# Optimization experiments

Hardware: AMD Instinct MI355X
Metric: run time of the kernel (lower is better)

The kernel has to match this reference:

```python
import jax, jax.numpy as jnp
import numpy as np

IN_FEATURES_LS = (32, 64, 128, 256)
OUT_FEATURES = 1024
B, T = 16, 4096


def setup_inputs() -> dict:
    key = jax.random.key(0)
    k_x, k_idx, k_w, k_b = jax.random.split(key, 4)
    n = len(IN_FEATURES_LS)
    x = jax.random.normal(k_x, (B, T, OUT_FEATURES), dtype=jnp.float32)
    # per-row declared feature size, drawn from the configured list
    branch_idx = jax.random.randint(k_idx, (B, T), 0, n)
    in_feat_size = jnp.array(IN_FEATURES_LS, dtype=jnp.int32)[branch_idx]
    # kaiming_uniform_(a=sqrt(5)) on (n, out, out): fan_in = out, bound = 1/sqrt(fan_in)
    bound_w = 1.0 / np.sqrt(OUT_FEATURES)
    weight = jax.random.uniform(k_w, (n, OUT_FEATURES, OUT_FEATURES), dtype=jnp.float32,
                                minval=-bound_w, maxval=bound_w)
    bound_b = 1.0 / np.sqrt(OUT_FEATURES)
    bias = jax.random.uniform(k_b, (n, OUT_FEATURES), dtype=jnp.float32,
                              minval=-bound_b, maxval=bound_b)
    return {"x": x, "in_feat_size": in_feat_size, "weight": weight, "bias": bias}


def reference(x, in_feat_size, weight, bias):
    # Loop over the small fixed set of feature-size branches (matches original).
    out = jnp.zeros(x.shape[:-1] + (OUT_FEATURES,), dtype=x.dtype)
    for idx, feat_size in enumerate(IN_FEATURES_LS):
        mask = (in_feat_size == feat_size)[..., None].astype(x.dtype)  # [B,T,1]
        y = jnp.einsum('oi,bti->bto', weight[idx], x) + bias[idx]
        out = out + mask * y
    return out
```

## Files before the change

### kernel.cpp

```cpp
#include <hip/hip_runtime.h>
#include <hip/hip_bf16.h>

#define OUTF 1024
#define NROWS 65536
#define NBR 4
#define BM 128
#define BN 128
#define BK 64
#define LDT 72

typedef __attribute__((ext_vector_type(8))) short short8;
typedef __attribute__((ext_vector_type(4))) float f32x4;

__device__ inline unsigned short f2bf(float f) {
    return __builtin_bit_cast(unsigned short, (__bf16)f);
}

__device__ inline void gload_lds16(const void* g, void* l) {
    __builtin_amdgcn_global_load_lds(
        (const __attribute__((address_space(1))) void*)g,
        (__attribute__((address_space(3))) void*)l, 16, 0, 0);
}

__global__ void k_count(const int* __restrict__ feat, int* __restrict__ cnt) {
    __shared__ int lc[NBR];
    int tid = threadIdx.x;
    if (tid < NBR) lc[tid] = 0;
    __syncthreads();
    int r = blockIdx.x * 256 + tid;
    int b = 26 - __clz(feat[r]);
    atomicAdd(&lc[b], 1);
    __syncthreads();
    if (tid < NBR && lc[tid]) atomicAdd(&cnt[tid], lc[tid]);
}

__global__ void k_prefix(int* __restrict__ ws) {
    if (threadIdx.x == 0) {
        int s = 0;
        for (int b = 0; b < NBR; b++) { ws[4 + b] = s; s += ws[b]; ws[8 + b] = 0; }
    }
}

__global__ void k_fill(const int* __restrict__ feat, int* __restrict__ ws,
                       int* __restrict__ rowlist) {
    int tid = threadIdx.x;
    int lane = tid & 63;
    int r = blockIdx.x * 256 + tid;
    int b = 26 - __clz(feat[r]);
    #pragma unroll
    for (int bb = 0; bb < NBR; bb++) {
        unsigned long long mask = __ballot(b == bb);
        int leader = __ffsll((long long)mask) - 1;
        int cntw = __popcll(mask);
        int basepos = 0;
        if (lane == leader) basepos = atomicAdd(&ws[8 + bb], cntw);
        basepos = __shfl(basepos, leader < 0 ? 0 : leader);
        if (b == bb) {
            int prefix = __popcll(mask & ((1ull << lane) - 1ull));
            rowlist[ws[4 + bb] + basepos + prefix] = r;
        }
    }
}

__global__ void k_convw(const float* __restrict__ w, unsigned short* __restrict__ wb) {
    int i = ((int)blockIdx.x * 256 + (int)threadIdx.x) * 4;
    const float4 v = *reinterpret_cast<const float4*>(w + i);
    ushort4 o;
    o.x = f2bf(v.x); o.y = f2bf(v.y); o.z = f2bf(v.z); o.w = f2bf(v.w);
    *reinterpret_cast<ushort4*>(wb + i) = o;
}

__global__ void k_convx(const float* __restrict__ x, const int* __restrict__ rowlist,
                        unsigned short* __restrict__ xb) {
    int idx = ((int)blockIdx.x * 256 + (int)threadIdx.x) << 3;
    int row = idx >> 10;
    int col = idx & (OUTF - 1);
    int src = rowlist[row];
    const float4* s = reinterpret_cast<const float4*>(x + (size_t)src * OUTF + col);
    float4 v0 = s[0], v1 = s[1];
    short8 o;
    o[0] = (short)f2bf(v0.x); o[1] = (short)f2bf(v0.y);
    o[2] = (short)f2bf(v0.z); o[3] = (short)f2bf(v0.w);
    o[4] = (short)f2bf(v1.x); o[5] = (short)f2bf(v1.y);
    o[6] = (short)f2bf(v1.z); o[7] = (short)f2bf(v1.w);
    *reinterpret_cast<short8*>(xb + idx) = o;
}

__global__ __launch_bounds__(256, 3)
void k_gemm2(const unsigned short* __restrict__ xb,
             const unsigned short* __restrict__ wb,
             const float* __restrict__ bias,
             const int* __restrict__ ws_i,
             const int* __restrict__ rowlist,
             float* __restrict__ out) {
    __shared__ unsigned short As[BM][BK];
    __shared__ unsigned short Bs[BN][BK];

    const int nwg = (int)gridDim.x;
    const int d = (int)blockIdx.x;
    const int wg = (d & 7) * (nwg >> 3) + (d >> 3);
    const int mtile = wg >> 3;
    const int ntile = wg & 7;

    int branch = -1, lt = 0, cnt = 0, rbase = 0;
    int t = mtile;
    #pragma unroll
    for (int b = 0; b < NBR; b++) {
        if (branch < 0) {
            int c = ws_i[b];
            int nt = (c + BM - 1) >> 7;
            if (t < nt) { branch = b; lt = t; cnt = c; rbase = ws_i[4 + b]; }
            else t -= nt;
        }
    }
    if (branch < 0) return;

    const int tid = threadIdx.x;
    const int lane = tid & 63;
    const int w = tid >> 6;
    const int wm = (w & 1) << 6;
    const int wn = (w >> 1) << 6;
    const int n0 = ntile * BN;
    const int row0 = rbase + lt * BM;

    const int lr = lane >> 3;
    const int lc = (lane & 7) << 3;
    const unsigned short* gA = xb + (size_t)(row0 + w * 32 + lr) * OUTF + lc;
    const unsigned short* gB = wb + ((size_t)branch << 20) + (size_t)(n0 + w * 32 + lr) * OUTF + lc;
    unsigned short* lA = &As[w * 32][0];
    unsigned short* lB = &Bs[w * 32][0];

    f32x4 acc[4][4];
    #pragma unroll
    for (int i = 0; i < 4; i++)
        #pragma unroll
        for (int j = 0; j < 4; j++)
            acc[i][j] = (f32x4){0.f, 0.f, 0.f, 0.f};

    for (int k0 = 0; k0 < OUTF; k0 += BK) {
        #pragma unroll
        for (int i = 0; i < 4; i++) {
            gload_lds16(gA + (size_t)i * 8 * OUTF + k0, lA + i * 8 * BK);
            gload_lds16(gB + (size_t)i * 8 * OUTF + k0, lB + i * 8 * BK);
        }
        __syncthreads();
        #pragma unroll
        for (int kk = 0; kk < BK; kk += 32) {
            const int krd = kk + (lane >> 4) * 8;
            short8 af[4], bfr[4];
            #pragma unroll
            for (int i = 0; i < 4; i++)
                af[i] = *reinterpret_cast<const short8*>(&As[wm + i * 16 + (lane & 15)][krd]);
            #pragma unroll
            for (int i = 0; i < 4; i++)
                bfr[i] = *reinterpret_cast<const short8*>(&Bs[wn + i * 16 + (lane & 15)][krd]);
            #pragma unroll
            for (int i = 0; i < 4; i++)
                #pragma unroll
                for (int j = 0; j < 4; j++)
                    acc[i][j] = __builtin_amdgcn_mfma_f32_16x16x32_bf16(af[i], bfr[j], acc[i][j], 0, 0, 0);
        }
        __syncthreads();
    }

    const int ccol = lane & 15;
    const int crow = (lane >> 4) << 2;
    float bv[4];
    const float* bp = bias + branch * OUTF + n0 + wn;
    #pragma unroll
    for (int fn = 0; fn < 4; fn++) bv[fn] = bp[fn * 16 + ccol];
    #pragma unroll
    for (int fm = 0; fm < 4; fm++) {
        #pragma unroll
        for (int j = 0; j < 4; j++) {
            int gm = lt * BM + wm + fm * 16 + crow + j;
            if (gm < cnt) {
                int orow = rowlist[rbase + gm];
                float* orp = out + (size_t)orow * OUTF + n0 + wn;
                #pragma unroll
                for (int fn = 0; fn < 4; fn++)
                    orp[fn * 16 + ccol] = acc[fm][fn][j] + bv[fn];
            }
        }
    }
}

template <bool USE_WB>
__global__ __launch_bounds__(256, 3)
void k_gemm_fb(const float* __restrict__ x,
               const unsigned short* __restrict__ wb,
               const float* __restrict__ wf,
               const float* __restrict__ bias,
               const int* __restrict__ ws_i,
               const int* __restrict__ rowlist,
               float* __restrict__ out) {
    __shared__ unsigned short As[BM][LDT];
    __shared__ unsigned short Bs[BN][LDT];

    int t = (int)blockIdx.x;
    int branch = -1, ltile = 0, cnt = 0, rbase = 0;
    #pragma unroll
    for (int b = 0; b < NBR; b++) {
        if (branch < 0) {
            int c = ws_i[b];
            int nt = (c + BM - 1) >> 7;
            if (t < nt) { branch = b; ltile = t; cnt = c; rbase = ws_i[4 + b]; }
            else t -= nt;
        }
    }
    if (branch < 0) return;

    const int tid = threadIdx.x;
    const int lane = tid & 63;
    const int wid = tid >> 6;
    const int wm = (wid & 1) << 6;
    const int wn = (wid >> 1) << 6;
    const int n0 = (int)blockIdx.y * BN;

    const int srow = tid >> 1;
    const int scol = (tid & 1) << 5;

    const int gmrow = ltile * BM + srow;
    const int grow = (gmrow < cnt) ? rowlist[rbase + gmrow] : -1;
    const float* xsrc = x + (size_t)(grow < 0 ? 0 : grow) * OUTF + scol;
    const unsigned short* wbsrc = wb + ((size_t)branch << 20) + (size_t)(n0 + srow) * OUTF + scol;
    const float* wfsrc = wf + ((size_t)branch << 20) + (size_t)(n0 + srow) * OUTF + scol;

    f32x4 acc[4][4];
    #pragma unroll
    for (int i = 0; i < 4; i++)
        #pragma unroll
        for (int j = 0; j < 4; j++)
            acc[i][j] = (f32x4){0.f, 0.f, 0.f, 0.f};

    for (int k0 = 0; k0 < OUTF; k0 += BK) {
        {
            unsigned short* dst = &As[srow][scol];
            if (grow >= 0) {
                const float4* s4 = reinterpret_cast<const float4*>(xsrc + k0);
                #pragma unroll
                for (int i = 0; i < 8; i++) {
                    float4 v = s4[i];
                    ushort4 o;
                    o.x = f2bf(v.x); o.y = f2bf(v.y); o.z = f2bf(v.z); o.w = f2bf(v.w);
                    reinterpret_cast<ushort4*>(dst)[i] = o;
                }
            } else {
                ushort4 z; z.x = z.y = z.z = z.w = 0;
                #pragma unroll
                for (int i = 0; i < 8; i++) reinterpret_cast<ushort4*>(dst)[i] = z;
            }
        }
        {
            unsigned short* dst = &Bs[srow][scol];
            if (USE_WB) {
                const int4* s4 = reinterpret_cast<const int4*>(wbsrc + k0);
                #pragma unroll
                for (int i = 0; i < 4; i++) reinterpret_cast<int4*>(dst)[i] = s4[i];
            } else {
                const float4* s4 = reinterpret_cast<const float4*>(wfsrc + k0);
                #pragma unroll
                for (int i = 0; i < 8; i++) {
                    float4 v = s4[i];
                    ushort4 o;
                    o.x = f2bf(v.x); o.y = f2bf(v.y); o.z = f2bf(v.z); o.w = f2bf(v.w);
                    reinterpret_cast<ushort4*>(dst)[i] = o;
                }
            }
        }
        __syncthreads();
        #pragma unroll
        for (int kk = 0; kk < BK; kk += 32) {
            const int krd = kk + (lane >> 4) * 8;
            short8 af[4], bf_[4];
            #pragma unroll
            for (int i = 0; i < 4; i++)
                af[i] = *reinterpret_cast<const short8*>(&As[wm + i * 16 + (lane & 15)][krd]);
            #pragma unroll
            for (int i = 0; i < 4; i++)
                bf_[i] = *reinterpret_cast<const short8*>(&Bs[wn + i * 16 + (lane & 15)][krd]);
            #pragma unroll
            for (int i = 0; i < 4; i++)
                #pragma unroll
                for (int j = 0; j < 4; j++)
                    acc[i][j] = __builtin_amdgcn_mfma_f32_16x16x32_bf16(af[i], bf_[j], acc[i][j], 0, 0, 0);
        }
        __syncthreads();
    }

    const int ccol = lane & 15;
    const int crow = (lane >> 4) << 2;
    float bv[4];
    const float* bp = bias + branch * OUTF + n0 + wn;
    #pragma unroll
    for (int fn = 0; fn < 4; fn++) bv[fn] = bp[fn * 16 + ccol];
    #pragma unroll
    for (int fm = 0; fm < 4; fm++) {
        #pragma unroll
        for (int j = 0; j < 4; j++) {
            int gm = ltile * BM + wm + fm * 16 + crow + j;
            if (gm < cnt) {
                int orow = rowlist[rbase + gm];
                float* orp = out + (size_t)orow * OUTF + n0 + wn;
                #pragma unroll
                for (int fn = 0; fn < 4; fn++)
                    orp[fn * 16 + ccol] = acc[fm][fn][j] + bv[fn];
            }
        }
    }
}

extern "C" void kernel_launch(void* const* d_in, const int* in_sizes, int n_in,
                              void* d_out, int out_size, void* d_ws, size_t ws_size,
                              hipStream_t stream) {
    const float* x = (const float*)d_in[0];
    const int* feat = (const int*)d_in[1];
    const float* w = (const float*)d_in[2];
    const float* bias = (const float*)d_in[3];
    float* out = (float*)d_out;

    char* ws = (char*)d_ws;
    int* ws_i = (int*)ws;
    int* rowlist = (int*)(ws + 256);
    const size_t WB_OFF = (size_t)512 << 10;
    const size_t XB_OFF = (size_t)16 << 20;
    unsigned short* wb = (unsigned short*)(ws + WB_OFF);
    unsigned short* xb = (unsigned short*)(ws + XB_OFF);
    const size_t need_wb = WB_OFF + (size_t)NBR * OUTF * OUTF * 2;
    const size_t need_full = XB_OFF + (size_t)(NROWS + 128) * OUTF * 2;

    hipMemsetAsync(ws_i, 0, 64, stream);
    k_count<<<NROWS / 256, 256, 0, stream>>>(feat, ws_i);
    k_prefix<<<1, 64, 0, stream>>>(ws_i);
    k_fill<<<NROWS / 256, 256, 0, stream>>>(feat, ws_i, rowlist);

    if (ws_size >= need_full) {
        k_convw<<<(NBR * OUTF * OUTF) / (256 * 4), 256, 0, stream>>>(w, wb);
        k_convx<<<(NROWS * (OUTF / 8)) / 256, 256, 0, stream>>>(x, rowlist, xb);
        const int nwg = (NROWS / BM + NBR) * (OUTF / BN);
        k_gemm2<<<nwg, 256, 0, stream>>>(xb, wb, bias, ws_i, rowlist, out);
    } else {
        dim3 grid(NROWS / BM + NBR, OUTF / BN);
        if (ws_size >= need_wb) {
            k_convw<<<(NBR * OUTF * OUTF) / (256 * 4), 256, 0, stream>>>(w, wb);
            k_gemm_fb<true><<<grid, 256, 0, stream>>>(x, wb, w, bias, ws_i, rowlist, out);
        } else {
            k_gemm_fb<false><<<grid, 256, 0, stream>>>(x, wb, w, bias, ws_i, rowlist, out);
        }
    }
}
```

Before: 365.6 us.

## Fuse x bf16 conversion into a larger double-buffered 256x256 GEMM tile

Removes the separate gather-and-convert pass over x. The GEMM now loads fp32 rows through rowlist, converts them to bf16 in registers and writes them to swizzled LDS. Tiles grow to 256x256 with 512 threads and 128KB of dynamic LDS, double-buffered so the next K-slab loads while MFMAs run, with setprio around the MFMA phases. This saves a full write and read of the bf16 copy of x, at the cost of lower occupancy, heavier register pressure and more padding waste on the ragged per-branch tiles.

```diff
diff --git a/kernel.cpp b/kernel.cpp
--- a/kernel.cpp
+++ b/kernel.cpp
@@ -4,10 +4,6 @@
 #define OUTF 1024
 #define NROWS 65536
 #define NBR 4
-#define BM 128
-#define BN 128
-#define BK 64
-#define LDT 72
 
 typedef __attribute__((ext_vector_type(8))) short short8;
 typedef __attribute__((ext_vector_type(4))) float f32x4;
@@ -15,11 +11,18 @@
 __device__ inline unsigned short f2bf(float f) {
     return __builtin_bit_cast(unsigned short, (__bf16)f);
 }
-
 __device__ inline void gload_lds16(const void* g, void* l) {
     __builtin_amdgcn_global_load_lds(
         (const __attribute__((address_space(1))) void*)g,
         (__attribute__((address_space(3))) void*)l, 16, 0, 0);
+}
+__device__ inline short8 pack8(float4 a, float4 b) {
+    short8 o;
+    o[0] = (short)f2bf(a.x); o[1] = (short)f2bf(a.y);
+    o[2] = (short)f2bf(a.z); o[3] = (short)f2bf(a.w);
+    o[4] = (short)f2bf(b.x); o[5] = (short)f2bf(b.y);
+    o[6] = (short)f2bf(b.z); o[7] = (short)f2bf(b.w);
+    return o;
 }
 
 __global__ void k_count(const int* __restrict__ feat, int* __restrict__ cnt) {
@@ -70,47 +73,30 @@
     *reinterpret_cast<ushort4*>(wb + i) = o;
 }
 
-__global__ void k_convx(const float* __restrict__ x, const int* __restrict__ rowlist,
-                        unsigned short* __restrict__ xb) {
-    int idx = ((int)blockIdx.x * 256 + (int)threadIdx.x) << 3;
-    int row = idx >> 10;
-    int col = idx & (OUTF - 1);
-    int src = rowlist[row];
-    const float4* s = reinterpret_cast<const float4*>(x + (size_t)src * OUTF + col);
-    float4 v0 = s[0], v1 = s[1];
-    short8 o;
-    o[0] = (short)f2bf(v0.x); o[1] = (short)f2bf(v0.y);
-    o[2] = (short)f2bf(v0.z); o[3] = (short)f2bf(v0.w);
-    o[4] = (short)f2bf(v1.x); o[5] = (short)f2bf(v1.y);
-    o[6] = (short)f2bf(v1.z); o[7] = (short)f2bf(v1.w);
-    *reinterpret_cast<short8*>(xb + idx) = o;
-}
-
-__global__ __launch_bounds__(256, 3)
-void k_gemm2(const unsigned short* __restrict__ xb,
+__global__ __launch_bounds__(512, 2)
+void k_gemm3(const float* __restrict__ x,
              const unsigned short* __restrict__ wb,
              const float* __restrict__ bias,
              const int* __restrict__ ws_i,
              const int* __restrict__ rowlist,
              float* __restrict__ out) {
-    __shared__ unsigned short As[BM][BK];
-    __shared__ unsigned short Bs[BN][BK];
-
+    extern __shared__ char lds[];
+
+    const int d = (int)blockIdx.x;
     const int nwg = (int)gridDim.x;
-    const int d = (int)blockIdx.x;
-    const int wg = (d & 7) * (nwg >> 3) + (d >> 3);
-    const int mtile = wg >> 3;
-    const int ntile = wg & 7;
+    const int work = (d & 7) * (nwg >> 3) + (d >> 3);
+    const int mtile = work >> 2;
+    const int ntile = work & 3;
 
     int branch = -1, lt = 0, cnt = 0, rbase = 0;
-    int t = mtile;
+    int t_ = mtile;
     #pragma unroll
     for (int b = 0; b < NBR; b++) {
         if (branch < 0) {
             int c = ws_i[b];
-            int nt = (c + BM - 1) >> 7;
-            if (t < nt) { branch = b; lt = t; cnt = c; rbase = ws_i[4 + b]; }
-            else t -= nt;
+            int nt = (c + 255) >> 8;
+            if (t_ < nt) { branch = b; lt = t_; cnt = c; rbase = ws_i[4 + b]; }
+            else t_ -= nt;
         }
     }
     if (branch < 0) return;
@@ -118,49 +104,140 @@
     const int tid = threadIdx.x;
     const int lane = tid & 63;
     const int w = tid >> 6;
-    const int wm = (w & 1) << 6;
-    const int wn = (w >> 1) << 6;
-    const int n0 = ntile * BN;
-    const int row0 = rbase + lt * BM;
-
-    const int lr = lane >> 3;
-    const int lc = (lane & 7) << 3;
-    const unsigned short* gA = xb + (size_t)(row0 + w * 32 + lr) * OUTF + lc;
-    const unsigned short* gB = wb + ((size_t)branch << 20) + (size_t)(n0 + w * 32 + lr) * OUTF + lc;
-    unsigned short* lA = &As[w * 32][0];
-    unsigned short* lB = &Bs[w * 32][0];
-
-    f32x4 acc[4][4];
-    #pragma unroll
-    for (int i = 0; i < 4; i++)
-        #pragma unroll
-        for (int j = 0; j < 4; j++)
-            acc[i][j] = (f32x4){0.f, 0.f, 0.f, 0.f};
-
-    for (int k0 = 0; k0 < OUTF; k0 += BK) {
+    const int wm = (w >> 2) * 128;
+    const int wn = (w & 3) * 64;
+    const int n0 = ntile * 256;
+
+    const float4* pA[4];
+    const char* gB[4];
+    const int row0 = rbase + lt * 256;
+    #pragma unroll
+    for (int i = 0; i < 4; i++) {
+        const int Dl = i * 8192 + w * 1024 + lane * 16;
+        const int row = Dl >> 7;
+        const int colb = (Dl & 127) ^ ((row & 7) << 4);
+        int idx = row0 + row;
+        int grow = rowlist[idx < NROWS ? idx : 0];
+        pA[i] = reinterpret_cast<const float4*>(x + (size_t)grow * OUTF + (colb >> 1));
+        gB[i] = reinterpret_cast<const char*>(wb + ((size_t)branch << 20) + (size_t)(n0 + row) * OUTF) + colb;
+    }
+
+    f32x4 acc[8][4];
+    #pragma unroll
+    for (int i = 0; i < 8; i++)
+        #pragma unroll
+        for (int j = 0; j < 4; j++) acc[i][j] = (f32x4){0.f, 0.f, 0.f, 0.f};
+
+    const int klane = (lane >> 4) << 4;
+    const int swz = (lane & 7) << 4;
+    const int arow = wm + (lane & 15);
+    const int brow = wn + (lane & 15);
+
+    {
+        char* A0 = lds;
+        char* B0 = lds + 32768;
         #pragma unroll
         for (int i = 0; i < 4; i++) {
-            gload_lds16(gA + (size_t)i * 8 * OUTF + k0, lA + i * 8 * BK);
-            gload_lds16(gB + (size_t)i * 8 * OUTF + k0, lB + i * 8 * BK);
-        }
+            float4 a0 = pA[i][0], a1 = pA[i][1];
+            const int Dl = i * 8192 + w * 1024 + lane * 16;
+            *reinterpret_cast<short8*>(A0 + Dl) = pack8(a0, a1);
+        }
+        #pragma unroll
+        for (int i = 0; i < 4; i++)
+            gload_lds16(gB[i], B0 + i * 8192 + w * 1024);
         __syncthreads();
-        #pragma unroll
-        for (int kk = 0; kk < BK; kk += 32) {
-            const int krd = kk + (lane >> 4) * 8;
-            short8 af[4], bfr[4];
+    }
+
+    short8 af[8], bfr[2];
+    int cur = 0;
+
+    for (int t = 0; t < 16; ++t) {
+        const int nb = cur ^ 1;
+        const bool st = (t < 15);
+        char* Ac = lds + cur * 65536;
+        char* Bc = Ac + 32768;
+        char* An = lds + nb * 65536;
+        char* Bn = An + 32768;
+        float4 ra[4][2];
+
+        if (st) {
             #pragma unroll
-            for (int i = 0; i < 4; i++)
-                af[i] = *reinterpret_cast<const short8*>(&As[wm + i * 16 + (lane & 15)][krd]);
+            for (int i = 0; i < 4; i++) {
+                ra[i][0] = pA[i][(t + 1) * 16];
+                ra[i][1] = pA[i][(t + 1) * 16 + 1];
+            }
+            gload_lds16(gB[0] + (t + 1) * 128, Bn + 0 * 8192 + w * 1024);
+            gload_lds16(gB[1] + (t + 1) * 128, Bn + 1 * 8192 + w * 1024);
+        }
+        #pragma unroll
+        for (int fm = 0; fm < 8; fm++)
+            af[fm] = *reinterpret_cast<const short8*>(Ac + (arow + fm * 16) * 128 + (klane ^ swz));
+        #pragma unroll
+        for (int fj = 0; fj < 2; fj++)
+            bfr[fj] = *reinterpret_cast<const short8*>(Bc + (brow + fj * 16) * 128 + (klane ^ swz));
+        __builtin_amdgcn_s_barrier();
+        __builtin_amdgcn_s_setprio(1);
+        #pragma unroll
+        for (int fm = 0; fm < 8; fm++) {
+            acc[fm][0] = __builtin_amdgcn_mfma_f32_16x16x32_bf16(af[fm], bfr[0], acc[fm][0], 0, 0, 0);
+            acc[fm][1] = __builtin_amdgcn_mfma_f32_16x16x32_bf16(af[fm], bfr[1], acc[fm][1], 0, 0, 0);
+        }
+        __builtin_amdgcn_s_setprio(0);
+        __builtin_amdgcn_s_barrier();
+
+        if (st) {
+            gload_lds16(gB[2] + (t + 1) * 128, Bn + 2 * 8192 + w * 1024);
+            gload_lds16(gB[3] + (t + 1) * 128, Bn + 3 * 8192 + w * 1024);
+        }
+        #pragma unroll
+        for (int fj = 0; fj < 2; fj++)
+            bfr[fj] = *reinterpret_cast<const short8*>(Bc + (brow + 32 + fj * 16) * 128 + (klane ^ swz));
+        __builtin_amdgcn_s_barrier();
+        __builtin_amdgcn_s_setprio(1);
+        #pragma unroll
+        for (int fm = 0; fm < 8; fm++) {
+            acc[fm][2] = __builtin_amdgcn_mfma_f32_16x16x32_bf16(af[fm], bfr[0], acc[fm][2], 0, 0, 0);
+            acc[fm][3] = __builtin_amdgcn_mfma_f32_16x16x32_bf16(af[fm], bfr[1], acc[fm][3], 0, 0, 0);
+        }
+        __builtin_amdgcn_s_setprio(0);
+        __builtin_amdgcn_s_barrier();
+
+        if (st) {
             #pragma unroll
-            for (int i = 0; i < 4; i++)
-                bfr[i] = *reinterpret_cast<const short8*>(&Bs[wn + i * 16 + (lane & 15)][krd]);
-            #pragma unroll
-            for (int i = 0; i < 4; i++)
-                #pragma unroll
-                for (int j = 0; j < 4; j++)
-                    acc[i][j] = __builtin_amdgcn_mfma_f32_16x16x32_bf16(af[i], bfr[j], acc[i][j], 0, 0, 0);
-        }
+            for (int i = 0; i < 4; i++) {
+                const int Dl = i * 8192 + w * 1024 + lane * 16;
+                *reinterpret_cast<short8*>(An + Dl) = pack8(ra[i][0], ra[i][1]);
+            }
+        }
+        #pragma unroll
+        for (int fm = 0; fm < 8; fm++)
+            af[fm] = *reinterpret_cast<const short8*>(Ac + (arow + fm * 16) * 128 + ((64 | klane) ^ swz));
+        #pragma unroll
+        for (int fj = 0; fj < 2; fj++)
+            bfr[fj] = *reinterpret_cast<const short8*>(Bc + (brow + fj * 16) * 128 + ((64 | klane) ^ swz));
+        __builtin_amdgcn_s_barrier();
+        __builtin_amdgcn_s_setprio(1);
+        #pragma unroll
+        for (int fm = 0; fm < 8; fm++) {
+            acc[fm][0] = __builtin_amdgcn_mfma_f32_16x16x32_bf16(af[fm], bfr[0], acc[fm][0], 0, 0, 0);
+            acc[fm][1] = __builtin_amdgcn_mfma_f32_16x16x32_bf16(af[fm], bfr[1], acc[fm][1], 0, 0, 0);
+        }
+        __builtin_amdgcn_s_setprio(0);
+        __builtin_amdgcn_s_barrier();
+
+        #pragma unroll
+        for (int fj = 0; fj < 2; fj++)
+            bfr[fj] = *reinterpret_cast<const short8*>(Bc + (brow + 32 + fj * 16) * 128 + ((64 | klane) ^ swz));
+        __builtin_amdgcn_s_barrier();
+        __builtin_amdgcn_s_setprio(1);
+        #pragma unroll
+        for (int fm = 0; fm < 8; fm++) {
+            acc[fm][2] = __builtin_amdgcn_mfma_f32_16x16x32_bf16(af[fm], bfr[0], acc[fm][2], 0, 0, 0);
+            acc[fm][3] = __builtin_amdgcn_mfma_f32_16x16x32_bf16(af[fm], bfr[1], acc[fm][3], 0, 0, 0);
+        }
+        __builtin_amdgcn_s_setprio(0);
         __syncthreads();
+        cur ^= 1;
     }
 
     const int ccol = lane & 15;
@@ -170,10 +247,10 @@
     #pragma unroll
     for (int fn = 0; fn < 4; fn++) bv[fn] = bp[fn * 16 + ccol];
     #pragma unroll
-    for (int fm = 0; fm < 4; fm++) {
+    for (int fm = 0; fm < 8; fm++) {
         #pragma unroll
         for (int j = 0; j < 4; j++) {
-            int gm = lt * BM + wm + fm * 16 + crow + j;
+            int gm = lt * 256 + wm + fm * 16 + crow + j;
             if (gm < cnt) {
                 int orow = rowlist[rbase + gm];
                 float* orp = out + (size_t)orow * OUTF + n0 + wn;
@@ -194,8 +271,8 @@
                const int* __restrict__ ws_i,
                const int* __restrict__ rowlist,
                float* __restrict__ out) {
-    __shared__ unsigned short As[BM][LDT];
-    __shared__ unsigned short Bs[BN][LDT];
+    __shared__ unsigned short As[128][72];
+    __shared__ unsigned short Bs[128][72];
 
     int t = (int)blockIdx.x;
     int branch = -1, ltile = 0, cnt = 0, rbase = 0;
@@ -203,7 +280,7 @@
     for (int b = 0; b < NBR; b++) {
         if (branch < 0) {
             int c = ws_i[b];
-            int nt = (c + BM - 1) >> 7;
+            int nt = (c + 127) >> 7;
             if (t < nt) { branch = b; ltile = t; cnt = c; rbase = ws_i[4 + b]; }
             else t -= nt;
         }
@@ -215,12 +292,12 @@
     const int wid = tid >> 6;
     const int wm = (wid & 1) << 6;
     const int wn = (wid >> 1) << 6;
-    const int n0 = (int)blockIdx.y * BN;
+    const int n0 = (int)blockIdx.y * 128;
 
     const int srow = tid >> 1;
     const int scol = (tid & 1) << 5;
 
-    const int gmrow = ltile * BM + srow;
+    const int gmrow = ltile * 128 + srow;
     const int grow = (gmrow < cnt) ? rowlist[rbase + gmrow] : -1;
     const float* xsrc = x + (size_t)(grow < 0 ? 0 : grow) * OUTF + scol;
     const unsigned short* wbsrc = wb + ((size_t)branch << 20) + (size_t)(n0 + srow) * OUTF + scol;
@@ -233,7 +310,7 @@
         for (int j = 0; j < 4; j++)
             acc[i][j] = (f32x4){0.f, 0.f, 0.f, 0.f};
 
-    for (int k0 = 0; k0 < OUTF; k0 += BK) {
+    for (int k0 = 0; k0 < OUTF; k0 += 64) {
         {
             unsigned short* dst = &As[srow][scol];
             if (grow >= 0) {
@@ -270,7 +347,7 @@
         }
         __syncthreads();
         #pragma unroll
-        for (int kk = 0; kk < BK; kk += 32) {
+        for (int kk = 0; kk < 64; kk += 32) {
             const int krd = kk + (lane >> 4) * 8;
             short8 af[4], bf_[4];
             #pragma unroll
@@ -298,7 +375,7 @@
     for (int fm = 0; fm < 4; fm++) {
         #pragma unroll
         for (int j = 0; j < 4; j++) {
-            int gm = ltile * BM + wm + fm * 16 + crow + j;
+            int gm = ltile * 128 + wm + fm * 16 + crow + j;
             if (gm < cnt) {
                 int orow = rowlist[rbase + gm];
                 float* orp = out + (size_t)orow * OUTF + n0 + wn;
@@ -323,29 +400,22 @@
     int* ws_i = (int*)ws;
     int* rowlist = (int*)(ws + 256);
     const size_t WB_OFF = (size_t)512 << 10;
-    const size_t XB_OFF = (size_t)16 << 20;
     unsigned short* wb = (unsigned short*)(ws + WB_OFF);
-    unsigned short* xb = (unsigned short*)(ws + XB_OFF);
     const size_t need_wb = WB_OFF + (size_t)NBR * OUTF * OUTF * 2;
-    const size_t need_full = XB_OFF + (size_t)(NROWS + 128) * OUTF * 2;
-
-    hipMemsetAsync(ws_i, 0, 64, stream);
+
+    (void)hipMemsetAsync(ws_i, 0, 64, stream);
     k_count<<<NROWS / 256, 256, 0, stream>>>(feat, ws_i);
     k_prefix<<<1, 64, 0, stream>>>(ws_i);
     k_fill<<<NROWS / 256, 256, 0, stream>>>(feat, ws_i, rowlist);
 
-    if (ws_size >= need_full) {
+    if (ws_size >= need_wb) {
         k_convw<<<(NBR * OUTF * OUTF) / (256 * 4), 256, 0, stream>>>(w, wb);
-        k_convx<<<(NROWS * (OUTF / 8)) / 256, 256, 0, stream>>>(x, rowlist, xb);
-        const int nwg = (NROWS / BM + NBR) * (OUTF / BN);
-        k_gemm2<<<nwg, 256, 0, stream>>>(xb, wb, bias, ws_i, rowlist, out);
+        const int nwg = (NROWS / 256 + NBR) * 4;
+        (void)hipFuncSetAttribute((const void*)k_gemm3,
+                                  hipFuncAttributeMaxDynamicSharedMemorySize, 131072);
+        k_gemm3<<<nwg, 512, 131072, stream>>>(x, wb, bias, ws_i, rowlist, out);
     } else {
-        dim3 grid(NROWS / BM + NBR, OUTF / BN);
-        if (ws_size >= need_wb) {
-            k_convw<<<(NBR * OUTF * OUTF) / (256 * 4), 256, 0, stream>>>(w, wb);
-            k_gemm_fb<true><<<grid, 256, 0, stream>>>(x, wb, w, bias, ws_i, rowlist, out);
-        } else {
-            k_gemm_fb<false><<<grid, 256, 0, stream>>>(x, wb, w, bias, ws_i, rowlist, out);
-        }
-    }
-}
+        dim3 grid(NROWS / 128 + NBR, OUTF / 128);
+        k_gemm_fb<false><<<grid, 256, 0, stream>>>(x, wb, w, bias, ws_i, rowlist, out);
+    }
+}
```

After: 399.7 us. +9.3%, slower.

## Fuse x bf16 conversion into a triple-buffered 128x256 GEMM with swizzled LDS

Applied to the files above, without the earlier changes.

Removes the separate k_convx pass. The GEMM now reads fp32 x rows directly through the row list, converts them to bf16 in registers and stores them into LDS. Weights are pre-swizzled during conversion so that LDS reads avoid bank conflicts. The GEMM uses a 128x256 tile with 512 threads, a 3-stage LDS ring with async global_load_lds for weights, explicit waitcnt/barriers and setprio around MFMA. This removes a full 256MB write-then-read of the converted x, at the cost of 144KB of dynamic LDS per block, which limits occupancy, and more complex synchronisation.

```diff
diff --git a/kernel.cpp b/kernel.cpp
--- a/kernel.cpp
+++ b/kernel.cpp
@@ -5,9 +5,13 @@
 #define NROWS 65536
 #define NBR 4
 #define BM 128
-#define BN 128
+#define BN 256
 #define BK 64
-#define LDT 72
+#define KITERS 16
+#define ABYTES 16384
+#define BBYTES 32768
+#define BUFB 49152
+#define NWG 2064
 
 typedef __attribute__((ext_vector_type(8))) short short8;
 typedef __attribute__((ext_vector_type(4))) float f32x4;
@@ -15,11 +19,18 @@
 __device__ inline unsigned short f2bf(float f) {
     return __builtin_bit_cast(unsigned short, (__bf16)f);
 }
-
 __device__ inline void gload_lds16(const void* g, void* l) {
     __builtin_amdgcn_global_load_lds(
         (const __attribute__((address_space(1))) void*)g,
         (__attribute__((address_space(3))) void*)l, 16, 0, 0);
+}
+__device__ inline short8 pack8(float4 a, float4 b) {
+    short8 o;
+    o[0] = (short)f2bf(a.x); o[1] = (short)f2bf(a.y);
+    o[2] = (short)f2bf(a.z); o[3] = (short)f2bf(a.w);
+    o[4] = (short)f2bf(b.x); o[5] = (short)f2bf(b.y);
+    o[6] = (short)f2bf(b.z); o[7] = (short)f2bf(b.w);
+    return o;
 }
 
 __global__ void k_count(const int* __restrict__ feat, int* __restrict__ cnt) {
@@ -62,105 +73,151 @@
     }
 }
 
-__global__ void k_convw(const float* __restrict__ w, unsigned short* __restrict__ wb) {
-    int i = ((int)blockIdx.x * 256 + (int)threadIdx.x) * 4;
-    const float4 v = *reinterpret_cast<const float4*>(w + i);
-    ushort4 o;
-    o.x = f2bf(v.x); o.y = f2bf(v.y); o.z = f2bf(v.z); o.w = f2bf(v.w);
-    *reinterpret_cast<ushort4*>(wb + i) = o;
-}
-
-__global__ void k_convx(const float* __restrict__ x, const int* __restrict__ rowlist,
-                        unsigned short* __restrict__ xb) {
-    int idx = ((int)blockIdx.x * 256 + (int)threadIdx.x) << 3;
-    int row = idx >> 10;
-    int col = idx & (OUTF - 1);
-    int src = rowlist[row];
-    const float4* s = reinterpret_cast<const float4*>(x + (size_t)src * OUTF + col);
+__global__ void k_convw(const float* __restrict__ w, unsigned short* __restrict__ wsw) {
+    int idx = (int)blockIdx.x * 256 + (int)threadIdx.x;
+    int branch = idx >> 17;
+    int rem = idx & 131071;
+    int n = rem >> 7;
+    int c8 = rem & 127;
+    int cb = c8 << 4;
+    int kw = cb >> 7;
+    int wb_ = cb & 127;
+    int src = kw * 64 + (((wb_) ^ ((n & 7) << 4)) >> 1);
+    const float4* s = reinterpret_cast<const float4*>(
+        w + ((size_t)branch << 20) + (size_t)n * OUTF + src);
     float4 v0 = s[0], v1 = s[1];
-    short8 o;
-    o[0] = (short)f2bf(v0.x); o[1] = (short)f2bf(v0.y);
-    o[2] = (short)f2bf(v0.z); o[3] = (short)f2bf(v0.w);
-    o[4] = (short)f2bf(v1.x); o[5] = (short)f2bf(v1.y);
-    o[6] = (short)f2bf(v1.z); o[7] = (short)f2bf(v1.w);
-    *reinterpret_cast<short8*>(xb + idx) = o;
-}
-
-__global__ __launch_bounds__(256, 3)
-void k_gemm2(const unsigned short* __restrict__ xb,
-             const unsigned short* __restrict__ wb,
+    char* dst = reinterpret_cast<char*>(wsw) + ((size_t)branch << 21) + (size_t)n * 2048 + cb;
+    *reinterpret_cast<short8*>(dst) = pack8(v0, v1);
+}
+
+__global__ __launch_bounds__(512, 2)
+void k_gemm4(const float* __restrict__ x,
+             const unsigned short* __restrict__ wsw,
              const float* __restrict__ bias,
              const int* __restrict__ ws_i,
              const int* __restrict__ rowlist,
              float* __restrict__ out) {
-    __shared__ unsigned short As[BM][BK];
-    __shared__ unsigned short Bs[BN][BK];
-
-    const int nwg = (int)gridDim.x;
+    extern __shared__ char lds[];
+
     const int d = (int)blockIdx.x;
-    const int wg = (d & 7) * (nwg >> 3) + (d >> 3);
-    const int mtile = wg >> 3;
-    const int ntile = wg & 7;
+    const int work = (d & 7) * (NWG >> 3) + (d >> 3);
+    const int mtile = work >> 2;
+    const int ntile = work & 3;
 
     int branch = -1, lt = 0, cnt = 0, rbase = 0;
-    int t = mtile;
+    int t_ = mtile;
     #pragma unroll
     for (int b = 0; b < NBR; b++) {
         if (branch < 0) {
             int c = ws_i[b];
-            int nt = (c + BM - 1) >> 7;
-            if (t < nt) { branch = b; lt = t; cnt = c; rbase = ws_i[4 + b]; }
-            else t -= nt;
+            int nt = (c + 127) >> 7;
+            if (t_ < nt) { branch = b; lt = t_; cnt = c; rbase = ws_i[4 + b]; }
+            else t_ -= nt;
         }
     }
     if (branch < 0) return;
 
     const int tid = threadIdx.x;
     const int lane = tid & 63;
-    const int w = tid >> 6;
-    const int wm = (w & 1) << 6;
-    const int wn = (w >> 1) << 6;
+    const int w8 = tid >> 6;
+    const int wm = (w8 >> 2) * 64;
+    const int wn = (w8 & 3) * 64;
     const int n0 = ntile * BN;
-    const int row0 = rbase + lt * BM;
-
-    const int lr = lane >> 3;
-    const int lc = (lane & 7) << 3;
-    const unsigned short* gA = xb + (size_t)(row0 + w * 32 + lr) * OUTF + lc;
-    const unsigned short* gB = wb + ((size_t)branch << 20) + (size_t)(n0 + w * 32 + lr) * OUTF + lc;
-    unsigned short* lA = &As[w * 32][0];
-    unsigned short* lB = &Bs[w * 32][0];
+
+    const int sarow = tid >> 2;
+    const int sacol = (tid & 3) << 4;
+    int aridx = rbase + lt * BM + sarow;
+    int agrow = rowlist[aridx < NROWS ? aridx : 0];
+    const float4* pa = reinterpret_cast<const float4*>(x + (size_t)agrow * OUTF + sacol);
+    const int awb0 = sarow * 128 + (((tid & 3) * 32) ^ ((sarow & 7) << 4));
+    const int awb1 = sarow * 128 + ((((tid & 3) * 32) + 16) ^ ((sarow & 7) << 4));
+
+    const char* gb[4];
+    #pragma unroll
+    for (int i = 0; i < 4; i++) {
+        int brow_ = i * 64 + (tid >> 3);
+        gb[i] = reinterpret_cast<const char*>(wsw) + ((size_t)branch << 21)
+                + (size_t)(n0 + brow_) * 2048 + ((tid & 7) << 4);
+    }
+    const int ldsoffB = tid * 16;
 
     f32x4 acc[4][4];
     #pragma unroll
     for (int i = 0; i < 4; i++)
         #pragma unroll
-        for (int j = 0; j < 4; j++)
-            acc[i][j] = (f32x4){0.f, 0.f, 0.f, 0.f};
-
-    for (int k0 = 0; k0 < OUTF; k0 += BK) {
-        #pragma unroll
-        for (int i = 0; i < 4; i++) {
-            gload_lds16(gA + (size_t)i * 8 * OUTF + k0, lA + i * 8 * BK);
-            gload_lds16(gB + (size_t)i * 8 * OUTF + k0, lB + i * 8 * BK);
-        }
-        __syncthreads();
-        #pragma unroll
-        for (int kk = 0; kk < BK; kk += 32) {
-            const int krd = kk + (lane >> 4) * 8;
-            short8 af[4], bfr[4];
-            #pragma unroll
-            for (int i = 0; i < 4; i++)
-                af[i] = *reinterpret_cast<const short8*>(&As[wm + i * 16 + (lane & 15)][krd]);
-            #pragma unroll
-            for (int i = 0; i < 4; i++)
-                bfr[i] = *reinterpret_cast<const short8*>(&Bs[wn + i * 16 + (lane & 15)][krd]);
+        for (int j = 0; j < 4; j++) acc[i][j] = (f32x4){0.f, 0.f, 0.f, 0.f};
+
+    const int swz = (lane & 7) << 4;
+    const int kq = (lane >> 4) << 4;
+    const int arowb = (wm + (lane & 15)) * 128;
+    const int browb = (wn + (lane & 15)) * 128;
+
+    float4 ra[4], rn[4];
+
+    #pragma unroll
+    for (int i = 0; i < 4; i++) ra[i] = pa[i];
+    #pragma unroll
+    for (int i = 0; i < 4; i++)
+        gload_lds16(gb[i], lds + ABYTES + i * 8192 + ldsoffB);
+    *reinterpret_cast<short8*>(lds + awb0) = pack8(ra[0], ra[1]);
+    *reinterpret_cast<short8*>(lds + awb1) = pack8(ra[2], ra[3]);
+    #pragma unroll
+    for (int i = 0; i < 4; i++) ra[i] = pa[16 + i];
+    #pragma unroll
+    for (int i = 0; i < 4; i++)
+        gload_lds16(gb[i] + 128, lds + BUFB + ABYTES + i * 8192 + ldsoffB);
+    asm volatile("s_waitcnt vmcnt(8) lgkmcnt(0)" ::: "memory");
+    __builtin_amdgcn_sched_barrier(0);
+    __builtin_amdgcn_s_barrier();
+    __builtin_amdgcn_sched_barrier(0);
+
+    short8 af[4], bf_[4];
+
+    for (int t = 0; t < KITERS; ++t) {
+        char* Ac = lds + (t % 3) * BUFB;
+        char* Bc = Ac + ABYTES;
+
+        if (t < KITERS - 2) {
+            #pragma unroll
+            for (int i = 0; i < 4; i++) rn[i] = pa[(t + 2) * 16 + i];
+            char* Bn = lds + ((t + 2) % 3) * BUFB + ABYTES;
+            #pragma unroll
+            for (int i = 0; i < 4; i++)
+                gload_lds16(gb[i] + (t + 2) * 128, Bn + i * 8192 + ldsoffB);
+        }
+        if (t < KITERS - 1) {
+            char* An = lds + ((t + 1) % 3) * BUFB;
+            *reinterpret_cast<short8*>(An + awb0) = pack8(ra[0], ra[1]);
+            *reinterpret_cast<short8*>(An + awb1) = pack8(ra[2], ra[3]);
+        }
+        #pragma unroll
+        for (int kh = 0; kh < 2; kh++) {
+            const int kb = kh * 64 + kq;
+            #pragma unroll
+            for (int i = 0; i < 4; i++)
+                af[i] = *reinterpret_cast<const short8*>(Ac + arowb + i * 2048 + (kb ^ swz));
+            #pragma unroll
+            for (int i = 0; i < 4; i++)
+                bf_[i] = *reinterpret_cast<const short8*>(Bc + browb + i * 2048 + (kb ^ swz));
+            __builtin_amdgcn_s_setprio(1);
             #pragma unroll
             for (int i = 0; i < 4; i++)
                 #pragma unroll
                 for (int j = 0; j < 4; j++)
-                    acc[i][j] = __builtin_amdgcn_mfma_f32_16x16x32_bf16(af[i], bfr[j], acc[i][j], 0, 0, 0);
-        }
-        __syncthreads();
+                    acc[i][j] = __builtin_amdgcn_mfma_f32_16x16x32_bf16(af[i], bf_[j], acc[i][j], 0, 0, 0);
+            __builtin_amdgcn_s_setprio(0);
+        }
+        #pragma unroll
+        for (int i = 0; i < 4; i++) ra[i] = rn[i];
+
+        if (t < KITERS - 2) {
+            asm volatile("s_waitcnt vmcnt(8) lgkmcnt(0)" ::: "memory");
+        } else {
+            asm volatile("s_waitcnt vmcnt(0) lgkmcnt(0)" ::: "memory");
+        }
+        __builtin_amdgcn_sched_barrier(0);
+        __builtin_amdgcn_s_barrier();
+        __builtin_amdgcn_sched_barrier(0);
     }
 
     const int ccol = lane & 15;
@@ -185,17 +242,15 @@
     }
 }
 
-template <bool USE_WB>
 __global__ __launch_bounds__(256, 3)
 void k_gemm_fb(const float* __restrict__ x,
-               const unsigned short* __restrict__ wb,
                const float* __restrict__ wf,
                const float* __restrict__ bias,
                const int* __restrict__ ws_i,
                const int* __restrict__ rowlist,
                float* __restrict__ out) {
-    __shared__ unsigned short As[BM][LDT];
-    __shared__ unsigned short Bs[BN][LDT];
+    __shared__ unsigned short As[128][72];
+    __shared__ unsigned short Bs[128][72];
 
     int t = (int)blockIdx.x;
     int branch = -1, ltile = 0, cnt = 0, rbase = 0;
@@ -203,7 +258,7 @@
     for (int b = 0; b < NBR; b++) {
         if (branch < 0) {
             int c = ws_i[b];
-            int nt = (c + BM - 1) >> 7;
+            int nt = (c + 127) >> 7;
             if (t < nt) { branch = b; ltile = t; cnt = c; rbase = ws_i[4 + b]; }
             else t -= nt;
         }
@@ -215,15 +270,14 @@
     const int wid = tid >> 6;
     const int wm = (wid & 1) << 6;
     const int wn = (wid >> 1) << 6;
-    const int n0 = (int)blockIdx.y * BN;
+    const int n0 = (int)blockIdx.y * 128;
 
     const int srow = tid >> 1;
     const int scol = (tid & 1) << 5;
 
-    const int gmrow = ltile * BM + srow;
+    const int gmrow = ltile * 128 + srow;
     const int grow = (gmrow < cnt) ? rowlist[rbase + gmrow] : -1;
     const float* xsrc = x + (size_t)(grow < 0 ? 0 : grow) * OUTF + scol;
-    const unsigned short* wbsrc = wb + ((size_t)branch << 20) + (size_t)(n0 + srow) * OUTF + scol;
     const float* wfsrc = wf + ((size_t)branch << 20) + (size_t)(n0 + srow) * OUTF + scol;
 
     f32x4 acc[4][4];
@@ -233,7 +287,7 @@
         for (int j = 0; j < 4; j++)
             acc[i][j] = (f32x4){0.f, 0.f, 0.f, 0.f};
 
-    for (int k0 = 0; k0 < OUTF; k0 += BK) {
+    for (int k0 = 0; k0 < OUTF; k0 += 64) {
         {
             unsigned short* dst = &As[srow][scol];
             if (grow >= 0) {
@@ -253,24 +307,18 @@
         }
         {
             unsigned short* dst = &Bs[srow][scol];
-            if (USE_WB) {
-                const int4* s4 = reinterpret_cast<const int4*>(wbsrc + k0);
-                #pragma unroll
-                for (int i = 0; i < 4; i++) reinterpret_cast<int4*>(dst)[i] = s4[i];
-            } else {
-                const float4* s4 = reinterpret_cast<const float4*>(wfsrc + k0);
-                #pragma unroll
-                for (int i = 0; i < 8; i++) {
-                    float4 v = s4[i];
-                    ushort4 o;
-                    o.x = f2bf(v.x); o.y = f2bf(v.y); o.z = f2bf(v.z); o.w = f2bf(v.w);
-                    reinterpret_cast<ushort4*>(dst)[i] = o;
-                }
+            const float4* s4 = reinterpret_cast<const float4*>(wfsrc + k0);
+            #pragma unroll
+            for (int i = 0; i < 8; i++) {
+                float4 v = s4[i];
+                ushort4 o;
+                o.x = f2bf(v.x); o.y = f2bf(v.y); o.z = f2bf(v.z); o.w = f2bf(v.w);
+                reinterpret_cast<ushort4*>(dst)[i] = o;
             }
         }
         __syncthreads();
         #pragma unroll
-        for (int kk = 0; kk < BK; kk += 32) {
+        for (int kk = 0; kk < 64; kk += 32) {
             const int krd = kk + (lane >> 4) * 8;
             short8 af[4], bf_[4];
             #pragma unroll
@@ -298,7 +346,7 @@
     for (int fm = 0; fm < 4; fm++) {
         #pragma unroll
         for (int j = 0; j < 4; j++) {
-            int gm = ltile * BM + wm + fm * 16 + crow + j;
+            int gm = ltile * 128 + wm + fm * 16 + crow + j;
             if (gm < cnt) {
                 int orow = rowlist[rbase + gm];
                 float* orp = out + (size_t)orow * OUTF + n0 + wn;
@@ -323,29 +371,21 @@
     int* ws_i = (int*)ws;
     int* rowlist = (int*)(ws + 256);
     const size_t WB_OFF = (size_t)512 << 10;
-    const size_t XB_OFF = (size_t)16 << 20;
-    unsigned short* wb = (unsigned short*)(ws + WB_OFF);
-    unsigned short* xb = (unsigned short*)(ws + XB_OFF);
-    const size_t need_wb = WB_OFF + (size_t)NBR * OUTF * OUTF * 2;
-    const size_t need_full = XB_OFF + (size_t)(NROWS + 128) * OUTF * 2;
-
-    hipMemsetAsync(ws_i, 0, 64, stream);
+    unsigned short* wsw = (unsigned short*)(ws + WB_OFF);
+    const size_t need = WB_OFF + (size_t)NBR * OUTF * OUTF * 2;
+
+    (void)hipMemsetAsync(ws_i, 0, 64, stream);
     k_count<<<NROWS / 256, 256, 0, stream>>>(feat, ws_i);
     k_prefix<<<1, 64, 0, stream>>>(ws_i);
     k_fill<<<NROWS / 256, 256, 0, stream>>>(feat, ws_i, rowlist);
 
-    if (ws_size >= need_full) {
-        k_convw<<<(NBR * OUTF * OUTF) / (256 * 4), 256, 0, stream>>>(w, wb);
-        k_convx<<<(NROWS * (OUTF / 8)) / 256, 256, 0, stream>>>(x, rowlist, xb);
-        const int nwg = (NROWS / BM + NBR) * (OUTF / BN);
-        k_gemm2<<<nwg, 256, 0, stream>>>(xb, wb, bias, ws_i, rowlist, out);
+    if (ws_size >= need) {
+        k_convw<<<2048, 256, 0, stream>>>(w, wsw);
+        (void)hipFuncSetAttribute((const void*)k_gemm4,
+                                  hipFuncAttributeMaxDynamicSharedMemorySize, 3 * BUFB);
+        k_gemm4<<<NWG, 512, 3 * BUFB, stream>>>(x, wsw, bias, ws_i, rowlist, out);
     } else {
-        dim3 grid(NROWS / BM + NBR, OUTF / BN);
-        if (ws_size >= need_wb) {
-            k_convw<<<(NBR * OUTF * OUTF) / (256 * 4), 256, 0, stream>>>(w, wb);
-            k_gemm_fb<true><<<grid, 256, 0, stream>>>(x, wb, w, bias, ws_i, rowlist, out);
-        } else {
-            k_gemm_fb<false><<<grid, 256, 0, stream>>>(x, wb, w, bias, ws_i, rowlist, out);
-        }
-    }
-}
+        dim3 grid(NROWS / 128 + NBR, OUTF / 128);
+        k_gemm_fb<<<grid, 256, 0, stream>>>(x, w, bias, ws_i, rowlist, out);
+    }
+}
```

Measured after the change: 358.9 us. Within noise of the previous version (-1.8%).
